# Kernel tuning notes

Measured on AMD Instinct MI355X. Metric: run time of the kernel, lower is better.

The kernel has to match this reference:

```python
import jax, jax.numpy as jnp
import numpy as np

NUM_SEQ, B, T, F, S, OUT = 4, 256, 64, 32, 512, 1


def setup_inputs() -> dict:
    key = jax.random.key(0)
    k = jax.random.split(key, 6)
    return {
        "inputs": jax.random.normal(k[0], (NUM_SEQ, B, T, F), dtype=jnp.float32),
        "W_cell": jax.random.normal(k[1], (NUM_SEQ, F + S, S), dtype=jnp.float32) * 0.05,
        "b_cell": jnp.zeros((NUM_SEQ, S), dtype=jnp.float32),
        "W_comb": jax.random.normal(k[2], (NUM_SEQ - 1, 2 * S, 1), dtype=jnp.float32) * 0.05,
        "b_comb": jnp.zeros((NUM_SEQ - 1, 1), dtype=jnp.float32),
        "W_out": jax.random.normal(k[3], (S, OUT), dtype=jnp.float32) * 0.05,
    }


def reference(inputs, W_cell, b_cell, W_comb, b_comb, W_out):
    # inputs: [num_seq, B, T, F]. Lanes are processed sequentially; lane i>0
    # gates its running state against lane i-1's stored per-step states.
    num_seq, bsz = inputs.shape[0], inputs.shape[1]
    state_size = W_cell.shape[-1]
    prev_states = None  # [T, B, S] states of previous lane
    final_states = []
    for i in range(num_seq):
        xs = jnp.swapaxes(inputs[i], 0, 1)  # [T, B, F]
        Wc, bc = W_cell[i], b_cell[i]
        h0 = jnp.zeros((bsz, state_size), dtype=inputs.dtype)
        if i == 0:
            def step(h, xt, Wc=Wc, bc=bc):
                h_new = jnp.tanh(jnp.concatenate([xt, h], axis=-1) @ Wc + bc)
                return h_new, h_new
            _, states = jax.lax.scan(step, h0, xs)
        else:
            Wg, bg = W_comb[i - 1], b_comb[i - 1]
            def step(h, x, Wc=Wc, bc=bc, Wg=Wg, bg=bg):
                xt, ph = x
                w = jax.nn.sigmoid(jnp.concatenate([h, ph], axis=-1) @ Wg + bg)  # [B,1]
                hc = w * h + (1.0 - w) * ph
                h_new = jnp.tanh(jnp.concatenate([xt, hc], axis=-1) @ Wc + bc)
                return h_new, h_new
            _, states = jax.lax.scan(step, h0, (xs, prev_states))
        prev_states = states  # [T, B, S]
        final_states.append(states[-1])
    final = jnp.concatenate(final_states, axis=0)  # [num_seq*B, S]
    out = final @ W_out  # no bias, matching tf.layers.dense(use_bias=False)
    return out.reshape(-1, num_seq, W_out.shape[1])  # [B, num_seq, OUT]
```

## Files before the change

### kernel.cpp

```cpp
#include <hip/hip_runtime.h>
#include <math.h>

#define NSEQ 4
#define BATCH 256
#define T 64
#define FIN 32
#define S 512
#define KTOT 544

#define NT 512
#define NWG 256
#define RPG 16
#define SW 128
#define DEPTH 4
#define NKT 17

#define RING_SZ  (4ull * DEPTH * BATCH * S)
#define OUTP_OFF RING_SZ
#define CTL_OFF  (RING_SZ + 16384ull)

#define FLAG_MAGIC 0x13572468u

#define AS 552

typedef __attribute__((ext_vector_type(8))) short short8;
typedef __attribute__((ext_vector_type(4))) float f32x4;
typedef __attribute__((ext_vector_type(4))) unsigned u32x4;

__device__ __forceinline__ unsigned short bf_hi(float f) {
  return (unsigned short)(__float_as_uint(f) >> 16);
}
__device__ __forceinline__ float bf_hi_f(float f) {
  return __uint_as_float(__float_as_uint(f) & 0xFFFF0000u);
}
__device__ __forceinline__ unsigned umin4(u32x4 v) {
  unsigned a = v[0] < v[1] ? v[0] : v[1];
  unsigned b = v[2] < v[3] ? v[2] : v[3];
  return a < b ? a : b;
}

__device__ __forceinline__ void cstoreu_glb(unsigned* p, unsigned v) {
  asm volatile("global_store_dword %0, %1, off sc0 sc1" :: "v"(p), "v"(v) : "memory");
}
__device__ __forceinline__ void cstore4_glb(unsigned* p, u32x4 v) {
  asm volatile("global_store_dwordx4 %0, %1, off sc0 sc1" :: "v"(p), "v"(v) : "memory");
}
__device__ __forceinline__ unsigned cldu_glb(const unsigned* p) {
  unsigned v;
  asm volatile("global_load_dword %0, %1, off sc0 sc1\n\ts_waitcnt vmcnt(0)"
               : "=v"(v) : "v"(p) : "memory");
  return v;
}
__device__ __forceinline__ u32x4 cld4_glb(const unsigned* p) {
  u32x4 v;
  asm volatile("global_load_dwordx4 %0, %1, off sc0 sc1\n\ts_waitcnt vmcnt(0)"
               : "=v"(v) : "v"(p) : "memory");
  return v;
}
__device__ __forceinline__ void cld3x4_glb(u32x4* a, u32x4* b, u32x4* c,
                                           const unsigned* pa, const unsigned* pb,
                                           const unsigned* pc) {
  asm volatile(
      "global_load_dwordx4 %0, %3, off sc0 sc1\n\t"
      "global_load_dwordx4 %1, %4, off sc0 sc1\n\t"
      "global_load_dwordx4 %2, %5, off sc0 sc1\n\t"
      "s_waitcnt vmcnt(0)"
      : "=&v"(*a), "=&v"(*b), "=&v"(*c)
      : "v"(pa), "v"(pb), "v"(pc) : "memory");
}
__device__ __forceinline__ void cstore1(float* p, float v) {
  asm volatile("global_store_dword %0, %1, off sc0 sc1" :: "v"(p), "v"(v) : "memory");
}
__device__ __forceinline__ float cload1(const float* p) {
  float v;
  asm volatile("global_load_dword %0, %1, off sc0 sc1\n\ts_waitcnt vmcnt(0)"
               : "=v"(v) : "v"(p) : "memory");
  return v;
}
__device__ __forceinline__ void cload_row(float4* d, const float* p) {
  asm volatile(
      "global_load_dwordx4 %0, %4, off sc0 sc1\n\t"
      "global_load_dwordx4 %1, %4, off offset:512 sc0 sc1\n\t"
      "global_load_dwordx4 %2, %4, off offset:1024 sc0 sc1\n\t"
      "global_load_dwordx4 %3, %4, off offset:1536 sc0 sc1\n\t"
      "s_waitcnt vmcnt(0)"
      : "=&v"(d[0]), "=&v"(d[1]), "=&v"(d[2]), "=&v"(d[3])
      : "v"(p) : "memory");
}
__device__ __forceinline__ void cload_row2(float4* h, float4* q,
                                           const float* ph, const float* pp) {
  asm volatile(
      "global_load_dwordx4 %0, %8, off sc0 sc1\n\t"
      "global_load_dwordx4 %1, %8, off offset:512 sc0 sc1\n\t"
      "global_load_dwordx4 %2, %8, off offset:1024 sc0 sc1\n\t"
      "global_load_dwordx4 %3, %8, off offset:1536 sc0 sc1\n\t"
      "global_load_dwordx4 %4, %9, off sc0 sc1\n\t"
      "global_load_dwordx4 %5, %9, off offset:512 sc0 sc1\n\t"
      "global_load_dwordx4 %6, %9, off offset:1024 sc0 sc1\n\t"
      "global_load_dwordx4 %7, %9, off offset:1536 sc0 sc1\n\t"
      "s_waitcnt vmcnt(0)"
      : "=&v"(h[0]), "=&v"(h[1]), "=&v"(h[2]), "=&v"(h[3]),
        "=&v"(q[0]), "=&v"(q[1]), "=&v"(q[2]), "=&v"(q[3])
      : "v"(ph), "v"(pp) : "memory");
}


extern "C" __global__ void __launch_bounds__(NT, 1)
rnn_mfma(const float* __restrict__ x,
         const float* __restrict__ Wcell,
         const float* __restrict__ bcell,
         const float* __restrict__ Wcomb,
         const float* __restrict__ bcomb,
         const float* __restrict__ Wout,
         float* __restrict__ out,
         float* __restrict__ ws)
{
  const int b    = blockIdx.x;
  const int o    = b >> 3;
  const int grp  = (b & 7) + 8 * (o >> 4);
  const int sub  = o & 15;
  const int lane = sub >> 2;
  const int sl   = sub & 3;
  const int gid  = lane * 16 + grp;
  const int r0 = grp * RPG, sb = sl * SW;
  const int tid = threadIdx.x;

  __shared__ __align__(16) unsigned short A1[RPG * AS];
  __shared__ __align__(16) unsigned short A2[RPG * AS];
  __shared__ float wg_lds[2 * S];
  __shared__ float obuf[128];
  __shared__ float fbuf[64];

  float* ring = ws;
  unsigned* ctl     = (unsigned*)(ws + CTL_OFF);
  unsigned* st_own  = ctl + gid * 64;
  unsigned* st_prod = ctl + (gid - 16) * 64;
  unsigned* st_cons = ctl + (gid + 16) * 64;
  unsigned* st_mine = st_own + sl;
  const unsigned* pp_poll = (lane > 0) ? st_prod : st_own;
  const unsigned* pc_poll = (lane < 3) ? st_cons : st_own;

  if (sl == 0 && tid == 0) {
    const u32x4 z = {0u, 0u, 0u, 0u};
    cstore4_glb(st_own, z);
    asm volatile("s_waitcnt vmcnt(0)" ::: "memory");
    cstoreu_glb(st_own + 32, FLAG_MAGIC);
  }
  if (tid == 0) {
    #pragma unroll
    for (int l = 0; l < 4; ++l) {
      const unsigned* f = ctl + (l * 16 + grp) * 64 + 32;
      while (cldu_glb(f) != FLAG_MAGIC) __builtin_amdgcn_s_sleep(1);
    }
  }

  const float* Wc = Wcell + (size_t)lane * KTOT * S;
  const int wl = tid & 63, wt = tid >> 6;
  const int bn = wl & 15, q = wl >> 4;
  const int ncol = sb + wt * 16 + bn;
  short8 B1[NKT], B2[NKT];
  #pragma unroll
  for (int kt = 0; kt < NKT; ++kt) {
    short8 b1, b2;
    #pragma unroll
    for (int j = 0; j < 8; ++j) {
      const float w = Wc[(size_t)(kt * 32 + q * 8 + j) * S + ncol];
      b1[j] = (short)bf_hi(w);
      b2[j] = (short)bf_hi(w - bf_hi_f(w));
    }
    B1[kt] = b1; B2[kt] = b2;
  }
  const float bcv = bcell[lane * S + ncol];
  const float wov = Wout[ncol];
  for (int idx = tid; idx < 2 * S; idx += NT)
    wg_lds[idx] = (lane > 0) ? Wcomb[(size_t)(lane - 1) * 2 * S + idx] : 0.0f;
  const float bg = (lane > 0) ? bcomb[lane - 1] : 0.0f;
  const int grow = tid >> 5, gch = tid & 31;
  __syncthreads();

  float oacc[4] = {0.f, 0.f, 0.f, 0.f};

  for (int t = 0; t < T; ++t) {
    {
      const float f0 = x[(((size_t)lane * BATCH + r0 + grow) * T + t) * FIN + gch];
      A1[grow * AS + gch] = bf_hi(f0);
      A2[grow * AS + gch] = bf_hi(f0 - bf_hi_f(f0));
    }
    for (;;) {
      u32x4 so, sp, sc;
      cld3x4_glb(&so, &sp, &sc, st_own, pp_poll, pc_poll);
      bool ok = true;
      if (t > 0)                  ok &= (umin4(so) >= (unsigned)t);
      if (lane > 0)               ok &= (umin4(sp) >= (unsigned)(t + 1));
      if (lane < 3 && t >= DEPTH) ok &= (umin4(sc) >= (unsigned)(t - 3));
      if (ok) break;
      __builtin_amdgcn_s_sleep(1);
    }

    {
      const int row = grow;
      float4 hv[4], pv[4];
      const float* hb = ring + ((size_t)(lane * DEPTH + ((t - 1) & 3)) * BATCH + r0 + row) * S + gch * 4;
      const float* pb = ring + ((size_t)((lane - 1) * DEPTH + (t & 3)) * BATCH + r0 + row) * S + gch * 4;
      if (t > 0) {
        if (lane > 0) cload_row2(hv, pv, hb, pb);
        else          cload_row(hv, hb);
      } else {
        #pragma unroll
        for (int j = 0; j < 4; ++j) hv[j] = make_float4(0.f, 0.f, 0.f, 0.f);
        if (lane > 0) cload_row(pv, pb);
      }
      if (lane > 0) {
        float gs = 0.0f;
        #pragma unroll
        for (int j = 0; j < 4; ++j) {
          const float* wh = &wg_lds[j * 128 + gch * 4];
          const float* wp = wh + S;
          gs += hv[j].x * wh[0] + hv[j].y * wh[1] + hv[j].z * wh[2] + hv[j].w * wh[3];
          gs += pv[j].x * wp[0] + pv[j].y * wp[1] + pv[j].z * wp[2] + pv[j].w * wp[3];
        }
        gs += __shfl_xor(gs, 1);  gs += __shfl_xor(gs, 2);  gs += __shfl_xor(gs, 4);
        gs += __shfl_xor(gs, 8);  gs += __shfl_xor(gs, 16);
        const float w = 1.0f / (1.0f + __expf(-(gs + bg)));
        #pragma unroll
        for (int j = 0; j < 4; ++j) {
          hv[j].x = fmaf(w, hv[j].x - pv[j].x, pv[j].x);
          hv[j].y = fmaf(w, hv[j].y - pv[j].y, pv[j].y);
          hv[j].z = fmaf(w, hv[j].z - pv[j].z, pv[j].z);
          hv[j].w = fmaf(w, hv[j].w - pv[j].w, pv[j].w);
        }
      }
      #pragma unroll
      for (int j = 0; j < 4; ++j) {
        ushort4 h4, l4;
        h4.x = bf_hi(hv[j].x); l4.x = bf_hi(hv[j].x - bf_hi_f(hv[j].x));
        h4.y = bf_hi(hv[j].y); l4.y = bf_hi(hv[j].y - bf_hi_f(hv[j].y));
        h4.z = bf_hi(hv[j].z); l4.z = bf_hi(hv[j].z - bf_hi_f(hv[j].z));
        h4.w = bf_hi(hv[j].w); l4.w = bf_hi(hv[j].w - bf_hi_f(hv[j].w));
        const int ai = row * AS + 32 + j * 128 + gch * 4;
        *(ushort4*)&A1[ai] = h4;
        *(ushort4*)&A2[ai] = l4;
      }
    }
    __syncthreads();

    f32x4 acc = {0.f, 0.f, 0.f, 0.f};
    {
      const unsigned short* ar1 = &A1[bn * AS + q * 8];
      const unsigned short* ar2 = &A2[bn * AS + q * 8];
      #pragma unroll
      for (int kt = 0; kt < NKT; ++kt) {
        const short8 a1 = *(const short8*)(ar1 + kt * 32);
        const short8 a2 = *(const short8*)(ar2 + kt * 32);
        acc = __builtin_amdgcn_mfma_f32_16x16x32_bf16(a1, B1[kt], acc, 0, 0, 0);
        acc = __builtin_amdgcn_mfma_f32_16x16x32_bf16(a1, B2[kt], acc, 0, 0, 0);
        acc = __builtin_amdgcn_mfma_f32_16x16x32_bf16(a2, B1[kt], acc, 0, 0, 0);
      }
    }

    float* slot = ring + ((size_t)(lane * DEPTH + (t & 3)) * BATCH + r0) * S + sb;
    #pragma unroll
    for (int reg = 0; reg < 4; ++reg) {
      const float s2 = acc[reg] + bcv;
      const float aa = fabsf(s2), ee = __expf(2.0f * aa);
      const float tv = copysignf(1.0f - 2.0f / (ee + 1.0f), s2);
      cstore1(slot + (size_t)(q * 4 + reg) * S + wt * 16 + bn, tv);
      if (t == T - 1) oacc[reg] = tv * wov;
    }
    asm volatile("s_waitcnt vmcnt(0)" ::: "memory");
    __syncthreads();
    if (tid == 0) cstoreu_glb(st_mine, (unsigned)(t + 1));
  }

  #pragma unroll
  for (int reg = 0; reg < 4; ++reg) {
    float v = oacc[reg];
    v += __shfl_xor(v, 1); v += __shfl_xor(v, 2);
    v += __shfl_xor(v, 4); v += __shfl_xor(v, 8);
    if (bn == 0) obuf[wt * 16 + q * 4 + reg] = v;
  }
  __syncthreads();
  if (tid < 16) {
    float v = 0.0f;
    #pragma unroll
    for (int w = 0; w < 8; ++w) v += obuf[w * 16 + tid];
    cstore1(ws + OUTP_OFF + (size_t)((gid * 4 + sl) * 16 + tid), v);
  }
  asm volatile("s_waitcnt vmcnt(0)" ::: "memory");
  __syncthreads();
  if (tid == 0) cstoreu_glb(st_mine, (unsigned)(T + 1));
  if (sl == 0) {
    if (tid == 0)
      while (umin4(cld4_glb(st_own)) < (unsigned)(T + 1)) __builtin_amdgcn_s_sleep(1);
    __syncthreads();
    if (tid < 64) {
      const int sli = tid >> 4, r = tid & 15;
      fbuf[tid] = cload1(ws + OUTP_OFF + (size_t)((gid * 4 + sli) * 16 + r));
    }
    __syncthreads();
    if (tid < 16) {
      float s2 = 0.f;
      #pragma unroll
      for (int sli = 0; sli < 4; ++sli) s2 += fbuf[sli * 16 + tid];
      out[lane * BATCH + r0 + tid] = s2;
    }
  }
}

extern "C" void kernel_launch(void* const* d_in, const int* in_sizes, int n_in,
                              void* d_out, int out_size, void* d_ws, size_t ws_size,
                              hipStream_t stream) {
  (void)in_sizes; (void)n_in; (void)out_size; (void)ws_size;
  rnn_mfma<<<dim3(NWG), dim3(NT), 0, stream>>>(
      (const float*)d_in[0],
      (const float*)d_in[1],
      (const float*)d_in[2],
      (const float*)d_in[3],
      (const float*)d_in[4],
      (const float*)d_in[5],
      (float*)d_out,
      (float*)d_ws);
}
```

Measured before the change: 367.9 us.

## Replace per-step block barrier with per-wave ring-slot counters and early step signaling

Each wave now publishes its own completion counter per ring slot after storing its tanh outputs. Consumers poll those per-wave counters, reduced with a wave-wide min, instead of waiting for a block-level step counter that only advanced after a trailing __syncthreads. The step counter is now written right after the LDS staging barrier and serves only for ring-slot reuse (WAR) checks. The MFMA accumulation is also split into two independent accumulators to shorten the dependency chain. The startup handshake is reworked so each block sets its own flag and polls neighbours. The cost is more fine-grained flag traffic and a more complex, riskier memory-ordering protocol.

```diff
diff --git a/kernel.cpp b/kernel.cpp
--- a/kernel.cpp
+++ b/kernel.cpp
@@ -38,18 +38,24 @@
   unsigned b = v[2] < v[3] ? v[2] : v[3];
   return a < b ? a : b;
 }
+__device__ __forceinline__ bool alleq4(u32x4 v, unsigned m) {
+  return v[0] == m && v[1] == m && v[2] == m && v[3] == m;
+}
+__device__ __forceinline__ unsigned wave_umin(unsigned v) {
+  v = min(v, (unsigned)__shfl_xor((int)v, 1));
+  v = min(v, (unsigned)__shfl_xor((int)v, 2));
+  v = min(v, (unsigned)__shfl_xor((int)v, 4));
+  v = min(v, (unsigned)__shfl_xor((int)v, 8));
+  v = min(v, (unsigned)__shfl_xor((int)v, 16));
+  v = min(v, (unsigned)__shfl_xor((int)v, 32));
+  return v;
+}
 
 __device__ __forceinline__ void cstoreu_glb(unsigned* p, unsigned v) {
   asm volatile("global_store_dword %0, %1, off sc0 sc1" :: "v"(p), "v"(v) : "memory");
 }
 __device__ __forceinline__ void cstore4_glb(unsigned* p, u32x4 v) {
   asm volatile("global_store_dwordx4 %0, %1, off sc0 sc1" :: "v"(p), "v"(v) : "memory");
-}
-__device__ __forceinline__ unsigned cldu_glb(const unsigned* p) {
-  unsigned v;
-  asm volatile("global_load_dword %0, %1, off sc0 sc1\n\ts_waitcnt vmcnt(0)"
-               : "=v"(v) : "v"(p) : "memory");
-  return v;
 }
 __device__ __forceinline__ u32x4 cld4_glb(const unsigned* p) {
   u32x4 v;
@@ -57,17 +63,6 @@
                : "=v"(v) : "v"(p) : "memory");
   return v;
 }
-__device__ __forceinline__ void cld3x4_glb(u32x4* a, u32x4* b, u32x4* c,
-                                           const unsigned* pa, const unsigned* pb,
-                                           const unsigned* pc) {
-  asm volatile(
-      "global_load_dwordx4 %0, %3, off sc0 sc1\n\t"
-      "global_load_dwordx4 %1, %4, off sc0 sc1\n\t"
-      "global_load_dwordx4 %2, %5, off sc0 sc1\n\t"
-      "s_waitcnt vmcnt(0)"
-      : "=&v"(*a), "=&v"(*b), "=&v"(*c)
-      : "v"(pa), "v"(pb), "v"(pc) : "memory");
-}
 __device__ __forceinline__ void cstore1(float* p, float v) {
   asm volatile("global_store_dword %0, %1, off sc0 sc1" :: "v"(p), "v"(v) : "memory");
 }
@@ -77,18 +72,21 @@
                : "=v"(v) : "v"(p) : "memory");
   return v;
 }
-__device__ __forceinline__ void cload_row(float4* d, const float* p) {
+__device__ __forceinline__ void poll_cl(unsigned* hc, unsigned* pc,
+                                        u32x4* so, u32x4* sc,
+                                        const unsigned* phc, const unsigned* ppc,
+                                        const unsigned* pso, const unsigned* psc) {
   asm volatile(
-      "global_load_dwordx4 %0, %4, off sc0 sc1\n\t"
-      "global_load_dwordx4 %1, %4, off offset:512 sc0 sc1\n\t"
-      "global_load_dwordx4 %2, %4, off offset:1024 sc0 sc1\n\t"
-      "global_load_dwordx4 %3, %4, off offset:1536 sc0 sc1\n\t"
+      "global_load_dword %0, %4, off sc0 sc1\n\t"
+      "global_load_dword %1, %5, off sc0 sc1\n\t"
+      "global_load_dwordx4 %2, %6, off sc0 sc1\n\t"
+      "global_load_dwordx4 %3, %7, off sc0 sc1\n\t"
       "s_waitcnt vmcnt(0)"
-      : "=&v"(d[0]), "=&v"(d[1]), "=&v"(d[2]), "=&v"(d[3])
-      : "v"(p) : "memory");
-}
-__device__ __forceinline__ void cload_row2(float4* h, float4* q,
-                                           const float* ph, const float* pp) {
+      : "=&v"(*hc), "=&v"(*pc), "=&v"(*so), "=&v"(*sc)
+      : "v"(phc), "v"(ppc), "v"(pso), "v"(psc) : "memory");
+}
+__device__ __forceinline__ void ld_hp(float4* h, float4* p,
+                                      const float* ph, const float* pp) {
   asm volatile(
       "global_load_dwordx4 %0, %8, off sc0 sc1\n\t"
       "global_load_dwordx4 %1, %8, off offset:512 sc0 sc1\n\t"
@@ -100,8 +98,18 @@
       "global_load_dwordx4 %7, %9, off offset:1536 sc0 sc1\n\t"
       "s_waitcnt vmcnt(0)"
       : "=&v"(h[0]), "=&v"(h[1]), "=&v"(h[2]), "=&v"(h[3]),
-        "=&v"(q[0]), "=&v"(q[1]), "=&v"(q[2]), "=&v"(q[3])
+        "=&v"(p[0]), "=&v"(p[1]), "=&v"(p[2]), "=&v"(p[3])
       : "v"(ph), "v"(pp) : "memory");
+}
+__device__ __forceinline__ void cload_row(float4* d, const float* p) {
+  asm volatile(
+      "global_load_dwordx4 %0, %4, off sc0 sc1\n\t"
+      "global_load_dwordx4 %1, %4, off offset:512 sc0 sc1\n\t"
+      "global_load_dwordx4 %2, %4, off offset:1024 sc0 sc1\n\t"
+      "global_load_dwordx4 %3, %4, off offset:1536 sc0 sc1\n\t"
+      "s_waitcnt vmcnt(0)"
+      : "=&v"(d[0]), "=&v"(d[1]), "=&v"(d[2]), "=&v"(d[3])
+      : "v"(p) : "memory");
 }
 
 
@@ -134,23 +142,32 @@
   float* ring = ws;
   unsigned* ctl     = (unsigned*)(ws + CTL_OFF);
   unsigned* st_own  = ctl + gid * 64;
-  unsigned* st_prod = ctl + (gid - 16) * 64;
   unsigned* st_cons = ctl + (gid + 16) * 64;
   unsigned* st_mine = st_own + sl;
-  const unsigned* pp_poll = (lane > 0) ? st_prod : st_own;
-  const unsigned* pc_poll = (lane < 3) ? st_cons : st_own;
-
+  unsigned* flg_own  = st_own + 32;
+  unsigned* flg_prod = ctl + (gid - 16) * 64 + 32;
+  unsigned* flg_cons = st_cons + 32;
+  unsigned* can = ctl + 8192;
+  const unsigned* psc = (lane < 3) ? st_cons : st_own;
+
+  if (tid < 32) {
+    const int slot = tid >> 3, wv = tid & 7;
+    cstoreu_glb(can + (((lane * 4 + slot) * 16 + grp) * 32) + sl * 8 + wv, 0u);
+  }
   if (sl == 0 && tid == 0) {
     const u32x4 z = {0u, 0u, 0u, 0u};
     cstore4_glb(st_own, z);
-    asm volatile("s_waitcnt vmcnt(0)" ::: "memory");
-    cstoreu_glb(st_own + 32, FLAG_MAGIC);
-  }
+  }
+  asm volatile("s_waitcnt vmcnt(0)" ::: "memory");
+  __syncthreads();
   if (tid == 0) {
-    #pragma unroll
-    for (int l = 0; l < 4; ++l) {
-      const unsigned* f = ctl + (l * 16 + grp) * 64 + 32;
-      while (cldu_glb(f) != FLAG_MAGIC) __builtin_amdgcn_s_sleep(1);
+    cstoreu_glb(flg_own + sl, FLAG_MAGIC);
+    for (;;) {
+      bool ok = alleq4(cld4_glb(flg_own), FLAG_MAGIC);
+      if (lane > 0) ok &= alleq4(cld4_glb(flg_prod), FLAG_MAGIC);
+      if (lane < 3) ok &= alleq4(cld4_glb(flg_cons), FLAG_MAGIC);
+      if (ok) break;
+      __builtin_amdgcn_s_sleep(2);
     }
   }
 
@@ -176,6 +193,7 @@
     wg_lds[idx] = (lane > 0) ? Wcomb[(size_t)(lane - 1) * 2 * S + idx] : 0.0f;
   const float bg = (lane > 0) ? bcomb[lane - 1] : 0.0f;
   const int grow = tid >> 5, gch = tid & 31;
+  const int cpoll = tid & 31;
   __syncthreads();
 
   float oacc[4] = {0.f, 0.f, 0.f, 0.f};
@@ -186,30 +204,40 @@
       A1[grow * AS + gch] = bf_hi(f0);
       A2[grow * AS + gch] = bf_hi(f0 - bf_hi_f(f0));
     }
-    for (;;) {
-      u32x4 so, sp, sc;
-      cld3x4_glb(&so, &sp, &sc, st_own, pp_poll, pc_poll);
-      bool ok = true;
-      if (t > 0)                  ok &= (umin4(so) >= (unsigned)t);
-      if (lane > 0)               ok &= (umin4(sp) >= (unsigned)(t + 1));
-      if (lane < 3 && t >= DEPTH) ok &= (umin4(sc) >= (unsigned)(t - 3));
-      if (ok) break;
-      __builtin_amdgcn_s_sleep(1);
-    }
 
     {
-      const int row = grow;
+      const unsigned* phc = (t > 0)
+          ? can + (((lane * 4 + ((t - 1) & 3)) * 16 + grp) * 32) + cpoll
+          : st_own;
+      const unsigned* ppc = (lane > 0)
+          ? can + ((((lane - 1) * 4 + (t & 3)) * 16 + grp) * 32) + cpoll
+          : st_own;
+      for (;;) {
+        unsigned hc, pc; u32x4 so, sc;
+        poll_cl(&hc, &pc, &so, &sc, phc, ppc, st_own, psc);
+        bool ok = true;
+        if (t > 0)    ok &= (wave_umin(hc) >= (unsigned)t);
+        if (lane > 0) ok &= (wave_umin(pc) >= (unsigned)(t + 1));
+        if (t >= 4) {
+          ok &= ((int)umin4(so) >= t - 2);
+          if (lane < 3) ok &= ((int)umin4(sc) >= t - 3);
+        }
+        if (ok) break;
+        __builtin_amdgcn_s_sleep(1);
+      }
+
       float4 hv[4], pv[4];
-      const float* hb = ring + ((size_t)(lane * DEPTH + ((t - 1) & 3)) * BATCH + r0 + row) * S + gch * 4;
-      const float* pb = ring + ((size_t)((lane - 1) * DEPTH + (t & 3)) * BATCH + r0 + row) * S + gch * 4;
+      const float* hb = ring + ((size_t)(lane * DEPTH + ((t - 1) & 3)) * BATCH + r0 + grow) * S + gch * 4;
+      const float* pb = ring + ((size_t)((lane - 1) * DEPTH + (t & 3)) * BATCH + r0 + grow) * S + gch * 4;
       if (t > 0) {
-        if (lane > 0) cload_row2(hv, pv, hb, pb);
+        if (lane > 0) ld_hp(hv, pv, hb, pb);
         else          cload_row(hv, hb);
       } else {
         #pragma unroll
         for (int j = 0; j < 4; ++j) hv[j] = make_float4(0.f, 0.f, 0.f, 0.f);
         if (lane > 0) cload_row(pv, pb);
       }
+
       if (lane > 0) {
         float gs = 0.0f;
         #pragma unroll
@@ -237,14 +265,16 @@
         h4.y = bf_hi(hv[j].y); l4.y = bf_hi(hv[j].y - bf_hi_f(hv[j].y));
         h4.z = bf_hi(hv[j].z); l4.z = bf_hi(hv[j].z - bf_hi_f(hv[j].z));
         h4.w = bf_hi(hv[j].w); l4.w = bf_hi(hv[j].w - bf_hi_f(hv[j].w));
-        const int ai = row * AS + 32 + j * 128 + gch * 4;
+        const int ai = grow * AS + 32 + j * 128 + gch * 4;
         *(ushort4*)&A1[ai] = h4;
         *(ushort4*)&A2[ai] = l4;
       }
     }
     __syncthreads();
 
-    f32x4 acc = {0.f, 0.f, 0.f, 0.f};
+    if (tid == 0) cstoreu_glb(st_mine, (unsigned)(t + 1));
+
+    f32x4 acc0 = {0.f, 0.f, 0.f, 0.f}, acc1 = {0.f, 0.f, 0.f, 0.f};
     {
       const unsigned short* ar1 = &A1[bn * AS + q * 8];
       const unsigned short* ar2 = &A2[bn * AS + q * 8];
@@ -252,26 +282,37 @@
       for (int kt = 0; kt < NKT; ++kt) {
         const short8 a1 = *(const short8*)(ar1 + kt * 32);
         const short8 a2 = *(const short8*)(ar2 + kt * 32);
-        acc = __builtin_amdgcn_mfma_f32_16x16x32_bf16(a1, B1[kt], acc, 0, 0, 0);
-        acc = __builtin_amdgcn_mfma_f32_16x16x32_bf16(a1, B2[kt], acc, 0, 0, 0);
-        acc = __builtin_amdgcn_mfma_f32_16x16x32_bf16(a2, B1[kt], acc, 0, 0, 0);
-      }
-    }
-
-    float* slot = ring + ((size_t)(lane * DEPTH + (t & 3)) * BATCH + r0) * S + sb;
-    #pragma unroll
-    for (int reg = 0; reg < 4; ++reg) {
-      const float s2 = acc[reg] + bcv;
-      const float aa = fabsf(s2), ee = __expf(2.0f * aa);
-      const float tv = copysignf(1.0f - 2.0f / (ee + 1.0f), s2);
-      cstore1(slot + (size_t)(q * 4 + reg) * S + wt * 16 + bn, tv);
-      if (t == T - 1) oacc[reg] = tv * wov;
-    }
-    asm volatile("s_waitcnt vmcnt(0)" ::: "memory");
+        if (kt < 9) {
+          acc0 = __builtin_amdgcn_mfma_f32_16x16x32_bf16(a1, B1[kt], acc0, 0, 0, 0);
+          acc0 = __builtin_amdgcn_mfma_f32_16x16x32_bf16(a1, B2[kt], acc0, 0, 0, 0);
+          acc0 = __builtin_amdgcn_mfma_f32_16x16x32_bf16(a2, B1[kt], acc0, 0, 0, 0);
+        } else {
+          acc1 = __builtin_amdgcn_mfma_f32_16x16x32_bf16(a1, B1[kt], acc1, 0, 0, 0);
+          acc1 = __builtin_amdgcn_mfma_f32_16x16x32_bf16(a1, B2[kt], acc1, 0, 0, 0);
+          acc1 = __builtin_amdgcn_mfma_f32_16x16x32_bf16(a2, B1[kt], acc1, 0, 0, 0);
+        }
+      }
+    }
     __syncthreads();
-    if (tid == 0) cstoreu_glb(st_mine, (unsigned)(t + 1));
-  }
-
+
+    {
+      float* slot = ring + ((size_t)(lane * DEPTH + (t & 3)) * BATCH + r0) * S + sb;
+      #pragma unroll
+      for (int reg = 0; reg < 4; ++reg) {
+        const float s2 = acc0[reg] + acc1[reg] + bcv;
+        const float aa = fabsf(s2), ee = __expf(2.0f * aa);
+        const float tv = copysignf(1.0f - 2.0f / (ee + 1.0f), s2);
+        cstore1(slot + (size_t)(q * 4 + reg) * S + wt * 16 + bn, tv);
+        if (t == T - 1) oacc[reg] = tv * wov;
+      }
+      asm volatile("s_waitcnt vmcnt(0)" ::: "memory");
+      if (wl == 0)
+        cstoreu_glb(can + (((lane * 4 + (t & 3)) * 16 + grp) * 32) + sl * 8 + wt,
+                    (unsigned)(t + 1));
+    }
+  }
+
+  __syncthreads();
   #pragma unroll
   for (int reg = 0; reg < 4; ++reg) {
     float v = oacc[reg];
```

Result: slower. 393.8 us (+7.0%).

## Halve workgroups so each owns 256 columns, keep own state in LDS

Applied to the files above, without the earlier changes.

Each lane/row-group is now split across 2 workgroups instead of 4, so each workgroup computes 256 output columns with two MFMA accumulator chains and twice the resident B fragments in registers. The workgroup keeps its own half of the new state in LDS and reads only the sibling half and the previous lane's state from the global ring. The single per-group step counter is replaced by per-slot 'can read' counters plus a 'has consumed' counter, so a producer can advance once readers have taken the slot. The intent is to cut cross-workgroup global traffic and synchronisation per step. The cost is fewer workgroups (less parallelism over CUs), more register pressure from the doubled weight fragments, and more serial MFMA work per workgroup.

```diff
diff --git a/kernel.cpp b/kernel.cpp
--- a/kernel.cpp
+++ b/kernel.cpp
@@ -9,11 +9,12 @@
 #define KTOT 544
 
 #define NT 512
-#define NWG 256
+#define NWG 128
 #define RPG 16
-#define SW 128
+#define SW 256
 #define DEPTH 4
 #define NKT 17
+#define HLS 260
 
 #define RING_SZ  (4ull * DEPTH * BATCH * S)
 #define OUTP_OFF RING_SZ
@@ -33,23 +34,9 @@
 __device__ __forceinline__ float bf_hi_f(float f) {
   return __uint_as_float(__float_as_uint(f) & 0xFFFF0000u);
 }
-__device__ __forceinline__ unsigned umin4(u32x4 v) {
-  unsigned a = v[0] < v[1] ? v[0] : v[1];
-  unsigned b = v[2] < v[3] ? v[2] : v[3];
-  return a < b ? a : b;
-}
 
 __device__ __forceinline__ void cstoreu_glb(unsigned* p, unsigned v) {
   asm volatile("global_store_dword %0, %1, off sc0 sc1" :: "v"(p), "v"(v) : "memory");
-}
-__device__ __forceinline__ void cstore4_glb(unsigned* p, u32x4 v) {
-  asm volatile("global_store_dwordx4 %0, %1, off sc0 sc1" :: "v"(p), "v"(v) : "memory");
-}
-__device__ __forceinline__ unsigned cldu_glb(const unsigned* p) {
-  unsigned v;
-  asm volatile("global_load_dword %0, %1, off sc0 sc1\n\ts_waitcnt vmcnt(0)"
-               : "=v"(v) : "v"(p) : "memory");
-  return v;
 }
 __device__ __forceinline__ u32x4 cld4_glb(const unsigned* p) {
   u32x4 v;
@@ -57,17 +44,6 @@
                : "=v"(v) : "v"(p) : "memory");
   return v;
 }
-__device__ __forceinline__ void cld3x4_glb(u32x4* a, u32x4* b, u32x4* c,
-                                           const unsigned* pa, const unsigned* pb,
-                                           const unsigned* pc) {
-  asm volatile(
-      "global_load_dwordx4 %0, %3, off sc0 sc1\n\t"
-      "global_load_dwordx4 %1, %4, off sc0 sc1\n\t"
-      "global_load_dwordx4 %2, %5, off sc0 sc1\n\t"
-      "s_waitcnt vmcnt(0)"
-      : "=&v"(*a), "=&v"(*b), "=&v"(*c)
-      : "v"(pa), "v"(pb), "v"(pc) : "memory");
-}
 __device__ __forceinline__ void cstore1(float* p, float v) {
   asm volatile("global_store_dword %0, %1, off sc0 sc1" :: "v"(p), "v"(v) : "memory");
 }
@@ -76,6 +52,39 @@
   asm volatile("global_load_dword %0, %1, off sc0 sc1\n\ts_waitcnt vmcnt(0)"
                : "=v"(v) : "v"(p) : "memory");
   return v;
+}
+__device__ __forceinline__ void poll4(u32x4* a, u32x4* b, u32x4* c, u32x4* d,
+                                      const unsigned* pa, const unsigned* pb,
+                                      const unsigned* pc, const unsigned* pd) {
+  asm volatile(
+      "global_load_dwordx4 %0, %4, off sc0 sc1\n\t"
+      "global_load_dwordx4 %1, %5, off sc0 sc1\n\t"
+      "global_load_dwordx4 %2, %6, off sc0 sc1\n\t"
+      "global_load_dwordx4 %3, %7, off sc0 sc1\n\t"
+      "s_waitcnt vmcnt(0)"
+      : "=&v"(*a), "=&v"(*b), "=&v"(*c), "=&v"(*d)
+      : "v"(pa), "v"(pb), "v"(pc), "v"(pd) : "memory");
+}
+__device__ __forceinline__ void ld_s2p4(float4* s, float4* p,
+                                        const float* ps, const float* pp) {
+  asm volatile(
+      "global_load_dwordx4 %0, %6, off sc0 sc1\n\t"
+      "global_load_dwordx4 %1, %6, off offset:512 sc0 sc1\n\t"
+      "global_load_dwordx4 %2, %7, off sc0 sc1\n\t"
+      "global_load_dwordx4 %3, %7, off offset:512 sc0 sc1\n\t"
+      "global_load_dwordx4 %4, %7, off offset:1024 sc0 sc1\n\t"
+      "global_load_dwordx4 %5, %7, off offset:1536 sc0 sc1\n\t"
+      "s_waitcnt vmcnt(0)"
+      : "=&v"(s[0]), "=&v"(s[1]),
+        "=&v"(p[0]), "=&v"(p[1]), "=&v"(p[2]), "=&v"(p[3])
+      : "v"(ps), "v"(pp) : "memory");
+}
+__device__ __forceinline__ void ld_s2(float4* s, const float* ps) {
+  asm volatile(
+      "global_load_dwordx4 %0, %2, off sc0 sc1\n\t"
+      "global_load_dwordx4 %1, %2, off offset:512 sc0 sc1\n\t"
+      "s_waitcnt vmcnt(0)"
+      : "=&v"(s[0]), "=&v"(s[1]) : "v"(ps) : "memory");
 }
 __device__ __forceinline__ void cload_row(float4* d, const float* p) {
   asm volatile(
@@ -86,22 +95,6 @@
       "s_waitcnt vmcnt(0)"
       : "=&v"(d[0]), "=&v"(d[1]), "=&v"(d[2]), "=&v"(d[3])
       : "v"(p) : "memory");
-}
-__device__ __forceinline__ void cload_row2(float4* h, float4* q,
-                                           const float* ph, const float* pp) {
-  asm volatile(
-      "global_load_dwordx4 %0, %8, off sc0 sc1\n\t"
-      "global_load_dwordx4 %1, %8, off offset:512 sc0 sc1\n\t"
-      "global_load_dwordx4 %2, %8, off offset:1024 sc0 sc1\n\t"
-      "global_load_dwordx4 %3, %8, off offset:1536 sc0 sc1\n\t"
-      "global_load_dwordx4 %4, %9, off sc0 sc1\n\t"
-      "global_load_dwordx4 %5, %9, off offset:512 sc0 sc1\n\t"
-      "global_load_dwordx4 %6, %9, off offset:1024 sc0 sc1\n\t"
-      "global_load_dwordx4 %7, %9, off offset:1536 sc0 sc1\n\t"
-      "s_waitcnt vmcnt(0)"
-      : "=&v"(h[0]), "=&v"(h[1]), "=&v"(h[2]), "=&v"(h[3]),
-        "=&v"(q[0]), "=&v"(q[1]), "=&v"(q[2]), "=&v"(q[3])
-      : "v"(ph), "v"(pp) : "memory");
 }
 
 
@@ -117,68 +110,80 @@
 {
   const int b    = blockIdx.x;
   const int o    = b >> 3;
-  const int grp  = (b & 7) + 8 * (o >> 4);
-  const int sub  = o & 15;
-  const int lane = sub >> 2;
-  const int sl   = sub & 3;
+  const int hi   = o >> 3;
+  const int lane = (o >> 1) & 3;
+  const int sl   = o & 1;
+  const int grp  = (b & 7) + 8 * hi;
   const int gid  = lane * 16 + grp;
   const int r0 = grp * RPG, sb = sl * SW;
   const int tid = threadIdx.x;
 
   __shared__ __align__(16) unsigned short A1[RPG * AS];
   __shared__ __align__(16) unsigned short A2[RPG * AS];
+  __shared__ __align__(16) float h_lds[RPG * HLS];
   __shared__ float wg_lds[2 * S];
   __shared__ float obuf[128];
-  __shared__ float fbuf[64];
+  __shared__ float fbuf[16];
 
   float* ring = ws;
-  unsigned* ctl     = (unsigned*)(ws + CTL_OFF);
-  unsigned* st_own  = ctl + gid * 64;
-  unsigned* st_prod = ctl + (gid - 16) * 64;
-  unsigned* st_cons = ctl + (gid + 16) * 64;
-  unsigned* st_mine = st_own + sl;
-  const unsigned* pp_poll = (lane > 0) ? st_prod : st_own;
-  const unsigned* pc_poll = (lane < 3) ? st_cons : st_own;
-
-  if (sl == 0 && tid == 0) {
-    const u32x4 z = {0u, 0u, 0u, 0u};
-    cstore4_glb(st_own, z);
+  unsigned* ctl      = (unsigned*)(ws + CTL_OFF);
+  unsigned* st_own   = ctl + gid * 64;
+  unsigned* st_cons  = ctl + (gid + 16) * 64;
+  unsigned* flg_own  = st_own + 32;
+  unsigned* flg_prod = ctl + (gid - 16) * 64 + 32;
+  unsigned* flg_cons = st_cons + 32;
+  unsigned* can = ctl + 8192;
+  const unsigned* psc = (lane < 3) ? st_cons : st_own;
+
+  if (tid == 0) {
+    cstoreu_glb(st_own + sl, 0u);
+    #pragma unroll
+    for (int slot = 0; slot < 4; ++slot)
+      cstoreu_glb(can + ((lane * 4 + slot) * 16 + grp) * 32 + sl, 0u);
     asm volatile("s_waitcnt vmcnt(0)" ::: "memory");
-    cstoreu_glb(st_own + 32, FLAG_MAGIC);
-  }
-  if (tid == 0) {
-    #pragma unroll
-    for (int l = 0; l < 4; ++l) {
-      const unsigned* f = ctl + (l * 16 + grp) * 64 + 32;
-      while (cldu_glb(f) != FLAG_MAGIC) __builtin_amdgcn_s_sleep(1);
+    cstoreu_glb(flg_own + sl, FLAG_MAGIC);
+    for (;;) {
+      u32x4 f0 = cld4_glb(flg_own);
+      bool ok = (f0[0] == FLAG_MAGIC) && (f0[1] == FLAG_MAGIC);
+      if (lane > 0) { u32x4 fp = cld4_glb(flg_prod);
+                      ok &= (fp[0] == FLAG_MAGIC) && (fp[1] == FLAG_MAGIC); }
+      if (lane < 3) { u32x4 fc = cld4_glb(flg_cons);
+                      ok &= (fc[0] == FLAG_MAGIC) && (fc[1] == FLAG_MAGIC); }
+      if (ok) break;
+      __builtin_amdgcn_s_sleep(2);
     }
   }
 
   const float* Wc = Wcell + (size_t)lane * KTOT * S;
   const int wl = tid & 63, wt = tid >> 6;
   const int bn = wl & 15, q = wl >> 4;
-  const int ncol = sb + wt * 16 + bn;
-  short8 B1[NKT], B2[NKT];
+  const int ncolA = sb + wt * 32 + bn;
+  const int ncolB = ncolA + 16;
+  short8 B1a[NKT], B2a[NKT], B1b[NKT], B2b[NKT];
   #pragma unroll
   for (int kt = 0; kt < NKT; ++kt) {
-    short8 b1, b2;
+    short8 b1a, b2a, b1b, b2b;
     #pragma unroll
     for (int j = 0; j < 8; ++j) {
-      const float w = Wc[(size_t)(kt * 32 + q * 8 + j) * S + ncol];
-      b1[j] = (short)bf_hi(w);
-      b2[j] = (short)bf_hi(w - bf_hi_f(w));
-    }
-    B1[kt] = b1; B2[kt] = b2;
-  }
-  const float bcv = bcell[lane * S + ncol];
-  const float wov = Wout[ncol];
+      const float wA = Wc[(size_t)(kt * 32 + q * 8 + j) * S + ncolA];
+      const float wB = Wc[(size_t)(kt * 32 + q * 8 + j) * S + ncolB];
+      b1a[j] = (short)bf_hi(wA); b2a[j] = (short)bf_hi(wA - bf_hi_f(wA));
+      b1b[j] = (short)bf_hi(wB); b2b[j] = (short)bf_hi(wB - bf_hi_f(wB));
+    }
+    B1a[kt] = b1a; B2a[kt] = b2a; B1b[kt] = b1b; B2b[kt] = b2b;
+  }
+  const float bcvA = bcell[lane * S + ncolA];
+  const float bcvB = bcell[lane * S + ncolB];
+  const float wovA = Wout[ncolA];
+  const float wovB = Wout[ncolB];
   for (int idx = tid; idx < 2 * S; idx += NT)
     wg_lds[idx] = (lane > 0) ? Wcomb[(size_t)(lane - 1) * 2 * S + idx] : 0.0f;
   const float bg = (lane > 0) ? bcomb[lane - 1] : 0.0f;
   const int grow = tid >> 5, gch = tid & 31;
   __syncthreads();
 
-  float oacc[4] = {0.f, 0.f, 0.f, 0.f};
+  float oaccA[4] = {0.f, 0.f, 0.f, 0.f};
+  float oaccB[4] = {0.f, 0.f, 0.f, 0.f};
 
   for (int t = 0; t < T; ++t) {
     {
@@ -186,30 +191,46 @@
       A1[grow * AS + gch] = bf_hi(f0);
       A2[grow * AS + gch] = bf_hi(f0 - bf_hi_f(f0));
     }
-    for (;;) {
-      u32x4 so, sp, sc;
-      cld3x4_glb(&so, &sp, &sc, st_own, pp_poll, pc_poll);
-      bool ok = true;
-      if (t > 0)                  ok &= (umin4(so) >= (unsigned)t);
-      if (lane > 0)               ok &= (umin4(sp) >= (unsigned)(t + 1));
-      if (lane < 3 && t >= DEPTH) ok &= (umin4(sc) >= (unsigned)(t - 3));
-      if (ok) break;
-      __builtin_amdgcn_s_sleep(1);
-    }
 
     {
-      const int row = grow;
+      const unsigned* hcl = can + ((lane * 4 + ((t - 1) & 3)) * 16 + grp) * 32;
+      const unsigned* pcl = (lane > 0)
+          ? can + (((lane - 1) * 4 + (t & 3)) * 16 + grp) * 32
+          : st_own;
+      for (;;) {
+        u32x4 hc, pc, so, sc;
+        poll4(&hc, &pc, &so, &sc, hcl, pcl, st_own, psc);
+        bool ok = true;
+        if (t > 0)    ok &= ((int)hc[sl ^ 1] >= t);
+        if (lane > 0) ok &= ((int)pc[0] >= t + 1) && ((int)pc[1] >= t + 1);
+        if (t >= 4) {
+          ok &= ((int)so[sl ^ 1] >= t - 2);
+          if (lane < 3) ok &= ((int)sc[0] >= t - 3) && ((int)sc[1] >= t - 3);
+        }
+        if (ok) break;
+        __builtin_amdgcn_s_sleep(1);
+      }
+
       float4 hv[4], pv[4];
-      const float* hb = ring + ((size_t)(lane * DEPTH + ((t - 1) & 3)) * BATCH + r0 + row) * S + gch * 4;
-      const float* pb = ring + ((size_t)((lane - 1) * DEPTH + (t & 3)) * BATCH + r0 + row) * S + gch * 4;
+      const float* hbase = ring + ((size_t)(lane * DEPTH + ((t - 1) & 3)) * BATCH + r0 + grow) * S;
+      const float* pbase = ring + ((size_t)((lane - 1) * DEPTH + (t & 3)) * BATCH + r0 + grow) * S;
+      const float* sib = hbase + (sl ^ 1) * SW + gch * 4;
+      const float* pp  = pbase + gch * 4;
       if (t > 0) {
-        if (lane > 0) cload_row2(hv, pv, hb, pb);
-        else          cload_row(hv, hb);
+        float4 s2[2];
+        if (lane > 0) ld_s2p4(s2, pv, sib, pp);
+        else          ld_s2(s2, sib);
+        const int lb = grow * HLS + gch * 4;
+        const float4 own0 = *(const float4*)&h_lds[lb];
+        const float4 own1 = *(const float4*)&h_lds[lb + 128];
+        if (sl == 0) { hv[0] = own0;  hv[1] = own1;  hv[2] = s2[0]; hv[3] = s2[1]; }
+        else         { hv[0] = s2[0]; hv[1] = s2[1]; hv[2] = own0;  hv[3] = own1;  }
       } else {
         #pragma unroll
         for (int j = 0; j < 4; ++j) hv[j] = make_float4(0.f, 0.f, 0.f, 0.f);
-        if (lane > 0) cload_row(pv, pb);
-      }
+        if (lane > 0) cload_row(pv, pp);
+      }
+
       if (lane > 0) {
         float gs = 0.0f;
         #pragma unroll
@@ -237,14 +258,15 @@
         h4.y = bf_hi(hv[j].y); l4.y = bf_hi(hv[j].y - bf_hi_f(hv[j].y));
         h4.z = bf_hi(hv[j].z); l4.z = bf_hi(hv[j].z - bf_hi_f(hv[j].z));
         h4.w = bf_hi(hv[j].w); l4.w = bf_hi(hv[j].w - bf_hi_f(hv[j].w));
-        const int ai = row * AS + 32 + j * 128 + gch * 4;
+        const int ai = grow * AS + 32 + j * 128 + gch * 4;
         *(ushort4*)&A1[ai] = h4;
         *(ushort4*)&A2[ai] = l4;
       }
     }
     __syncthreads();
-
-    f32x4 acc = {0.f, 0.f, 0.f, 0.f};
+    if (tid == 0) cstoreu_glb(st_own + sl, (unsigned)(t + 1));
+
+    f32x4 accA = {0.f, 0.f, 0.f, 0.f}, accB = {0.f, 0.f, 0.f, 0.f};
     {
       const unsigned short* ar1 = &A1[bn * AS + q * 8];
       const unsigned short* ar2 = &A2[bn * AS + q * 8];
@@ -252,29 +274,42 @@
       for (int kt = 0; kt < NKT; ++kt) {
         const short8 a1 = *(const short8*)(ar1 + kt * 32);
         const short8 a2 = *(const short8*)(ar2 + kt * 32);
-        acc = __builtin_amdgcn_mfma_f32_16x16x32_bf16(a1, B1[kt], acc, 0, 0, 0);
-        acc = __builtin_amdgcn_mfma_f32_16x16x32_bf16(a1, B2[kt], acc, 0, 0, 0);
-        acc = __builtin_amdgcn_mfma_f32_16x16x32_bf16(a2, B1[kt], acc, 0, 0, 0);
-      }
-    }
-
-    float* slot = ring + ((size_t)(lane * DEPTH + (t & 3)) * BATCH + r0) * S + sb;
-    #pragma unroll
-    for (int reg = 0; reg < 4; ++reg) {
-      const float s2 = acc[reg] + bcv;
-      const float aa = fabsf(s2), ee = __expf(2.0f * aa);
-      const float tv = copysignf(1.0f - 2.0f / (ee + 1.0f), s2);
-      cstore1(slot + (size_t)(q * 4 + reg) * S + wt * 16 + bn, tv);
-      if (t == T - 1) oacc[reg] = tv * wov;
+        accA = __builtin_amdgcn_mfma_f32_16x16x32_bf16(a1, B1a[kt], accA, 0, 0, 0);
+        accB = __builtin_amdgcn_mfma_f32_16x16x32_bf16(a1, B1b[kt], accB, 0, 0, 0);
+        accA = __builtin_amdgcn_mfma_f32_16x16x32_bf16(a1, B2a[kt], accA, 0, 0, 0);
+        accB = __builtin_amdgcn_mfma_f32_16x16x32_bf16(a1, B2b[kt], accB, 0, 0, 0);
+        accA = __builtin_amdgcn_mfma_f32_16x16x32_bf16(a2, B1a[kt], accA, 0, 0, 0);
+        accB = __builtin_amdgcn_mfma_f32_16x16x32_bf16(a2, B1b[kt], accB, 0, 0, 0);
+      }
+    }
+
+    {
+      float* slotp = ring + ((size_t)(lane * DEPTH + (t & 3)) * BATCH + r0) * S + sb;
+      #pragma unroll
+      for (int reg = 0; reg < 4; ++reg) {
+        const float sA = accA[reg] + bcvA;
+        const float aA = fabsf(sA), eA = __expf(2.0f * aA);
+        const float tA = copysignf(1.0f - 2.0f / (eA + 1.0f), sA);
+        h_lds[(q * 4 + reg) * HLS + wt * 32 + bn] = tA;
+        cstore1(slotp + (size_t)(q * 4 + reg) * S + wt * 32 + bn, tA);
+        const float sB = accB[reg] + bcvB;
+        const float aB = fabsf(sB), eB = __expf(2.0f * aB);
+        const float tB = copysignf(1.0f - 2.0f / (eB + 1.0f), sB);
+        h_lds[(q * 4 + reg) * HLS + wt * 32 + 16 + bn] = tB;
+        cstore1(slotp + (size_t)(q * 4 + reg) * S + wt * 32 + 16 + bn, tB);
+        if (t == T - 1) { oaccA[reg] = tA * wovA; oaccB[reg] = tB * wovB; }
+      }
     }
     asm volatile("s_waitcnt vmcnt(0)" ::: "memory");
     __syncthreads();
-    if (tid == 0) cstoreu_glb(st_mine, (unsigned)(t + 1));
+    if (tid == 0)
+      cstoreu_glb(can + ((lane * 4 + (t & 3)) * 16 + grp) * 32 + sl,
+                  (unsigned)(t + 1));
   }
 
   #pragma unroll
   for (int reg = 0; reg < 4; ++reg) {
-    float v = oacc[reg];
+    float v = oaccA[reg] + oaccB[reg];
     v += __shfl_xor(v, 1); v += __shfl_xor(v, 2);
     v += __shfl_xor(v, 4); v += __shfl_xor(v, 8);
     if (bn == 0) obuf[wt * 16 + q * 4 + reg] = v;
@@ -284,25 +319,24 @@
     float v = 0.0f;
     #pragma unroll
     for (int w = 0; w < 8; ++w) v += obuf[w * 16 + tid];
-    cstore1(ws + OUTP_OFF + (size_t)((gid * 4 + sl) * 16 + tid), v);
+    fbuf[tid] = v;
+    cstore1(ws + OUTP_OFF + (size_t)((gid * 2 + sl) * 16 + tid), v);
   }
   asm volatile("s_waitcnt vmcnt(0)" ::: "memory");
   __syncthreads();
-  if (tid == 0) cstoreu_glb(st_mine, (unsigned)(T + 1));
+  if (tid == 0) cstoreu_glb(st_own + sl, (unsigned)(T + 1));
   if (sl == 0) {
-    if (tid == 0)
-      while (umin4(cld4_glb(st_own)) < (unsigned)(T + 1)) __builtin_amdgcn_s_sleep(1);
-    __syncthreads();
-    if (tid < 64) {
-      const int sli = tid >> 4, r = tid & 15;
-      fbuf[tid] = cload1(ws + OUTP_OFF + (size_t)((gid * 4 + sli) * 16 + r));
+    if (tid == 0) {
+      for (;;) {
+        u32x4 s = cld4_glb(st_own);
+        if ((int)s[1] >= T + 1) break;
+        __builtin_amdgcn_s_sleep(1);
+      }
     }
     __syncthreads();
     if (tid < 16) {
-      float s2 = 0.f;
-      #pragma unroll
-      for (int sli = 0; sli < 4; ++sli) s2 += fbuf[sli * 16 + tid];
-      out[lane * BATCH + r0 + tid] = s2;
+      const float sib = cload1(ws + OUTP_OFF + (size_t)((gid * 2 + 1) * 16 + tid));
+      out[lane * BATCH + r0 + tid] = fbuf[tid] + sib;
     }
   }
 }
```

Result: slower. 1.029 ms (+179.6%).
